# Optimization experiments

Hardware: AMD Instinct MI355X
Metric: run time of the kernel (lower is better)

## Reference

```python
import jax, jax.numpy as jnp
import numpy as np
from jax import lax

EPS = 1e-5

def conv3x3(x, w):
    # x: [B,C,H,W], w: [O,C,3,3]
    return lax.conv_general_dilated(x, w, (1, 1), ((1, 1), (1, 1)),
                                    dimension_numbers=("NCHW", "OIHW", "NCHW"))

def convbnrelu(x, w, bn):
    gamma, beta, mean, var = bn  # each [C]
    y = conv3x3(x, w)
    scale = (gamma / jnp.sqrt(var + EPS))[:, None, None]
    shift = (beta - mean * gamma / jnp.sqrt(var + EPS))[:, None, None]
    return jax.nn.relu(y * scale + shift)

def conv1x1(x, w, b):
    # w: [O,C,1,1], b: [O]
    return jnp.einsum("bchw,oc->bohw", x, w[:, :, 0, 0]) + b[:, None, None]

def pam(x, wb, bb, wc, bc, wd, bd, alpha, lfm=None):
    B, C, H, W = x.shape
    N = H * W
    q = conv1x1(x, wb, bb)
    k = conv1x1(x, wc, bc)
    v = conv1x1(x, wd, bd)
    if lfm is not None:  # VFAM: qkv flags all 1 -> multiply q, k, v
        q = q * lfm
        k = k * lfm
        v = v * lfm
    fb = q.reshape(B, -1, N).transpose(0, 2, 1)           # [B,N,Cq]
    fc = k.reshape(B, -1, N)                              # [B,Cq,N]
    attn = jax.nn.softmax(jnp.matmul(fb, fc), axis=-1)    # [B,N,N]
    fd = v.reshape(B, C, N)                               # [B,C,N]
    fe = jnp.matmul(fd, attn.transpose(0, 2, 1)).reshape(B, C, H, W)
    return alpha * fe + x

def cam(x, beta):
    B, C, H, W = x.shape
    N = H * W
    fa = x.reshape(B, C, N)
    attn = jnp.matmul(fa, fa.transpose(0, 2, 1))          # [B,C,C]
    attn = jnp.max(attn, axis=-1, keepdims=True) - attn
    attn = jax.nn.softmax(attn, axis=-1)
    fe = jnp.matmul(attn, fa).reshape(B, C, H, W)
    return beta * fe + x

def setup_inputs() -> dict:
    key = jax.random.key(0)
    ks = iter(jax.random.split(key, 64))
    B, Cin, H, W = 2, 2048, 64, 64
    Cmid = Cin // 4         # 512
    Cq = Cmid // 8          # 64
    nclass = 19

    def bn_pack(C):
        g = jnp.ones((C,)) + 0.1 * jax.random.normal(next(ks), (C,))
        b = 0.1 * jax.random.normal(next(ks), (C,))
        m = 0.1 * jax.random.normal(next(ks), (C,))
        v = jax.random.uniform(next(ks), (C,), minval=0.5, maxval=1.5)
        return jnp.stack([g, b, m, v])  # [4,C]

    def conv_w(O, I, kk):
        return jax.random.normal(next(ks), (O, I, kk, kk)) * (1.0 / np.sqrt(I * kk * kk))

    inp = {
        "x": jax.random.normal(next(ks), (B, Cin, H, W)),
        "loss_factor_map": jax.random.uniform(next(ks), (H, W)),
        "wp1": conv_w(Cmid, Cin, 3), "bnp1": bn_pack(Cmid),
        "wp2": conv_w(Cmid, Cmid, 3), "bnp2": bn_pack(Cmid),
        "wc1": conv_w(Cmid, Cin, 3), "bnc1": bn_pack(Cmid),
        "wc2": conv_w(Cmid, Cmid, 3), "bnc2": bn_pack(Cmid),
        "wv1": conv_w(Cmid, Cin, 3), "bnv1": bn_pack(Cmid),
        "wv2": conv_w(Cmid, Cmid, 3), "bnv2": bn_pack(Cmid),
        "pam_wb": conv_w(Cq, Cmid, 1), "pam_bb": jnp.zeros((Cq,)),
        "pam_wc": conv_w(Cq, Cmid, 1), "pam_bc": jnp.zeros((Cq,)),
        "pam_wd": conv_w(Cmid, Cmid, 1), "pam_bd": jnp.zeros((Cmid,)),
        "pam_alpha": 0.3 * jnp.ones((1,)),
        "cam_beta": 0.3 * jnp.ones((1,)),
        "vfam_wb": conv_w(Cq, Cmid, 1), "vfam_bb": jnp.zeros((Cq,)),
        "vfam_wc": conv_w(Cq, Cmid, 1), "vfam_bc": jnp.zeros((Cq,)),
        "vfam_wd": conv_w(Cmid, Cmid, 1), "vfam_bd": jnp.zeros((Cmid,)),
        "vfam_alpha": 0.3 * jnp.ones((1,)),
        "out_w": conv_w(nclass, Cmid, 1), "out_b": jnp.zeros((nclass,)),
        "p3_w": conv_w(nclass, Cmid, 1), "p3_b": jnp.zeros((nclass,)),
        "c3_w": conv_w(nclass, Cmid, 1), "c3_b": jnp.zeros((nclass,)),
    }
    return inp

def reference(x, loss_factor_map,
              wp1, bnp1, wp2, bnp2, wc1, bnc1, wc2, bnc2, wv1, bnv1, wv2, bnv2,
              pam_wb, pam_bb, pam_wc, pam_bc, pam_wd, pam_bd, pam_alpha,
              cam_beta,
              vfam_wb, vfam_bb, vfam_wc, vfam_bc, vfam_wd, vfam_bd, vfam_alpha,
              out_w, out_b, p3_w, p3_b, c3_w, c3_b):
    lfm = loss_factor_map[None, None, :, :]  # (1,1,H,W)
    # Position branch
    fp = convbnrelu(x, wp1, bnp1)
    fp = pam(fp, pam_wb, pam_bb, pam_wc, pam_bc, pam_wd, pam_bd, pam_alpha)
    fp = convbnrelu(fp, wp2, bnp2)
    # Channel branch
    fc = convbnrelu(x, wc1, bnc1)
    fc = cam(fc, cam_beta)
    fc = convbnrelu(fc, wc2, bnc2)
    # Visual-field branch (qkv_vfa_flag = [1,1,1])
    fv = convbnrelu(x, wv1, bnv1)
    fv = pam(fv, vfam_wb, vfam_bb, vfam_wc, vfam_bc, vfam_wd, vfam_bd, vfam_alpha, lfm=lfm)
    fv = convbnrelu(fv, wv2, bnv2)
    # Fusion + heads (Dropout in eval mode = identity)
    fusion = fp + fc + fv
    fusion_out = conv1x1(fusion, out_w, out_b)
    p_out = conv1x1(fp, p3_w, p3_b)
    c_out = conv1x1(fc, c3_w, c3_b)
    return (fusion_out, p_out, c_out)
```

## Files before the change

kernel.cpp:

```cpp
#include <hip/hip_runtime.h>

typedef unsigned short u16;
typedef short s16x8 __attribute__((ext_vector_type(8)));
typedef u16 u16x8 __attribute__((ext_vector_type(8)));
typedef u16 u16x4 __attribute__((ext_vector_type(4)));
typedef float f32x4 __attribute__((ext_vector_type(4)));

#define DEV __device__ __forceinline__

DEV float bf2f(u16 x) { unsigned v = ((unsigned)x) << 16; float f; __builtin_memcpy(&f, &v, 4); return f; }
DEV u16 f2bf(float f) { unsigned u; __builtin_memcpy(&u, &f, 4); u += 0x7FFFu + ((u >> 16) & 1u); return (u16)(u >> 16); }

DEV void gload16(const u16* g, u16* l) {
  __builtin_amdgcn_global_load_lds((const __attribute__((address_space(1))) void*)g,
                                   (__attribute__((address_space(3))) void*)l, 16, 0, 0);
}

__global__ void detect_dtype(const u16* __restrict__ x, int* __restrict__ flag) {
  int tid = threadIdx.x;
  float mx = 0.f;
  for (int i = tid; i < 4096; i += 256) mx = fmaxf(mx, fabsf(bf2f(x[i])));
  __shared__ float red[4];
  int wave = tid >> 6, lane = tid & 63;
  for (int off = 32; off; off >>= 1) mx = fmaxf(mx, __shfl_xor(mx, off));
  if (lane == 0) red[wave] = mx;
  __syncthreads();
  if (tid == 0) {
    mx = fmaxf(fmaxf(red[0], red[1]), fmaxf(red[2], red[3]));
    *flag = (mx > 1e4f) ? 1 : 0;
  }
}

struct CvBatch {
  const void* src[28];
  unsigned dstOff[28];
  unsigned n[28];
  unsigned chunkStart[29];
  int cnt;
};

__global__ __launch_bounds__(256) void convert_batch(CvBatch cb, u16* __restrict__ dstBase,
                                                     const int* __restrict__ flag) {
  const int isF = *flag;
  const unsigned bid = blockIdx.x;
  int j = 0;
  while (bid >= cb.chunkStart[j + 1]) ++j;
  const unsigned base = (bid - cb.chunkStart[j]) * 2048 + threadIdx.x * 8;
  const unsigned n = cb.n[j];
  if (base >= n) return;
  u16* dst = dstBase + cb.dstOff[j];
  const void* src = cb.src[j];
  if (base + 8 <= n) {
    u16x8 v;
    if (isF) {
      const float* f = (const float*)src;
#pragma unroll
      for (int k = 0; k < 8; ++k) v[k] = f2bf(f[base + k]);
    } else {
      v = *(const u16x8*)&((const u16*)src)[base];
    }
    *(u16x8*)&dst[base] = v;
  } else {
    for (unsigned i = base; i < n; ++i)
      dst[i] = isF ? f2bf(((const float*)src)[i]) : ((const u16*)src)[i];
  }
}

__global__ void bn_prep(const u16* __restrict__ cbn, float* __restrict__ out) {
  int w = blockIdx.x;
  const u16* bn = cbn + w * 2048;
  int c = threadIdx.x;
  float g = bf2f(bn[c]), be = bf2f(bn[512 + c]), m = bf2f(bn[1024 + c]), v = bf2f(bn[1536 + c]);
  float sc = g * rsqrtf(v + 1e-5f);
  out[w * 1024 + c] = sc;
  out[w * 1024 + 512 + c] = be - m * sc;
}

struct Repack3P { const void* src[3]; u16* dst[3]; };

__global__ __launch_bounds__(256) void repack_w3(Repack3P rp, int I, int Ishift,
                                                 const int* __restrict__ flag) {
  const int isF = *flag;
  const void* w = rp.src[blockIdx.z];
  u16* wr = rp.dst[blockIdx.z];
  size_t idx = ((size_t)blockIdx.x * 256 + threadIdx.x) * 8;
  int i0 = (int)(idx & (size_t)(I - 1));
  int t = (int)(idx >> Ishift);
  int o = t / 9, kk = t - o * 9;
  u16x8 v;
  if (isF) {
    const float* f = (const float*)w;
#pragma unroll
    for (int j = 0; j < 8; ++j) v[j] = f2bf(f[((size_t)o * I + i0 + j) * 9 + kk]);
  } else {
    const u16* bsrc = (const u16*)w;
#pragma unroll
    for (int j = 0; j < 8; ++j) v[j] = bsrc[((size_t)o * I + i0 + j) * 9 + kk];
  }
  *(u16x8*)&wr[idx] = v;
}

__global__ __launch_bounds__(256) void zero_border(u16* __restrict__ base, int CIN) {
  int p = blockIdx.x, b = blockIdx.y;
  int py, px;
  if (p < 66)       { py = 0;        px = p; }
  else if (p < 132) { py = 65;       px = p - 66; }
  else if (p < 196) { py = p - 131;  px = 0; }
  else              { py = p - 195;  px = 65; }
  u16* d = base + (((size_t)b * 66 + py) * 66 + px) * (size_t)CIN;
  for (int i = threadIdx.x * 8; i < CIN; i += 2048) {
    u16x8 z;
#pragma unroll
    for (int k = 0; k < 8; ++k) z[k] = 0;
    *(u16x8*)&d[i] = z;
  }
}

__global__ __launch_bounds__(256) void pad_nchw(const void* __restrict__ x, u16* __restrict__ xpad,
                                                const int* __restrict__ flag) {
  __shared__ u16 t[64][72];
  const int isF = *flag;
  int c0 = blockIdx.x * 64, h = blockIdx.y, b = blockIdx.z;
  int tid = threadIdx.x;
#pragma unroll
  for (int i = 0; i < 2; ++i) {
    int idx = i * 256 + tid;
    int cc = idx >> 3, ww = (idx & 7) * 8;
    size_t base = (((size_t)(b * 2048 + c0 + cc) * 64) + h) * 64 + ww;
    u16x8 v;
    if (isF) {
      const float* fx = (const float*)x;
#pragma unroll
      for (int j = 0; j < 8; ++j) v[j] = f2bf(fx[base + j]);
    } else {
      v = *(const u16x8*)&((const u16*)x)[base];
    }
    *(u16x8*)&t[cc][ww] = v;
  }
  __syncthreads();
#pragma unroll
  for (int i = 0; i < 2; ++i) {
    int idx = i * 256 + tid;
    int ww = idx >> 3, cc = (idx & 7) * 8;
    u16x8 v;
#pragma unroll
    for (int j = 0; j < 8; ++j) v[j] = t[cc + j][ww];
    *(u16x8*)&xpad[(((size_t)b * 66 + h + 1) * 66 + ww + 1) * 2048 + c0 + cc] = v;
  }
}

__global__ __launch_bounds__(256) void transpose64(const u16* __restrict__ src, u16* __restrict__ dst,
                                                   int R, int C) {
  __shared__ u16 t[64][72];
  int r0 = blockIdx.x * 64, c0 = blockIdx.y * 64;
  const u16* s = src + (size_t)blockIdx.z * R * C;
  u16* d = dst + (size_t)blockIdx.z * R * C;
  int tid = threadIdx.x;
#pragma unroll
  for (int i = 0; i < 2; ++i) {
    int idx = i * 256 + tid;
    int rr = idx >> 3, cc = (idx & 7) * 8;
    u16x8 v = *(const u16x8*)&s[(size_t)(r0 + rr) * C + c0 + cc];
    *(u16x8*)&t[rr][cc] = v;
  }
  __syncthreads();
#pragma unroll
  for (int i = 0; i < 2; ++i) {
    int idx = i * 256 + tid;
    int cc = idx >> 3, rr = (idx & 7) * 8;
    u16x8 v;
#pragma unroll
    for (int j = 0; j < 8; ++j) v[j] = t[rr + j][cc];
    *(u16x8*)&d[(size_t)(c0 + cc) * R + r0 + rr] = v;
  }
}

struct GemmP {
  const u16* A; const u16* B;
  long aBatch, bBatch;
  int M, N, K;
  u16* out; long outBatch; int ldOut;
  const u16* bias;
  const u16* rowscale;
  const u16* residual; long resBatch; int ldRes;
  const u16* alphaPtr;
  float* outF; long outFBatch;
  const u16* B2; const u16* bias2; u16* out2;
};

template <int BM, int BN, int EPI>
__global__ __launch_bounds__(256) void gemm_nt(GemmP p) {
  static_assert(EPI != 2 || BM >= BN, "EPI2 LDS bounce needs BM>=BN");
  constexpr int HB = (BM + BN) * 32;
  __shared__ __align__(16) u16 ls[2][HB];
  const int tid = threadIdx.x;
  int bz = blockIdx.z;
  const u16* Bsel = p.B;
  const u16* biasSel = p.bias;
  u16* outSel = p.out;
  if (EPI == 0 && p.out2) {
    const int h = gridDim.z >> 1;
    if (bz >= h) { bz -= h; Bsel = p.B2; biasSel = p.bias2; outSel = p.out2; }
  }
  const int m0 = blockIdx.x * BM, n0 = blockIdx.y * BN;
  const u16* A = p.A + (size_t)bz * p.aBatch;
  const u16* Bp = Bsel + (size_t)bz * p.bBatch;
  const int wave = tid >> 6, lane = tid & 63;
  const int quad = lane >> 4, r16 = lane & 15;
  const int wm = (wave >> 1) * (BM / 2), wn = (wave & 1) * (BN / 2);
  constexpr int TM = BM / 32, TN = BN / 32;
  f32x4 acc[TM][TN] = {};
  const int srow = tid >> 2, sch = (tid & 3) * 8;
  const int K = p.K;
  auto stage = [&](int buf, int k0) {
#pragma unroll
    for (int i = 0; i < BM / 64; ++i)
      gload16(&A[(size_t)(m0 + i * 64 + srow) * K + k0 + sch], &ls[buf][i * 2048 + wave * 512]);
#pragma unroll
    for (int i = 0; i < BN / 64; ++i)
      gload16(&Bp[(size_t)(n0 + i * 64 + srow) * K + k0 + sch],
              &ls[buf][BM * 32 + i * 2048 + wave * 512]);
  };
  stage(0, 0);
  __syncthreads();
  int cur = 0;
  for (int k0 = 0; k0 < K; k0 += 32) {
    if (k0 + 32 < K) stage(cur ^ 1, k0 + 32);
    const u16* lA = &ls[cur][0];
    const u16* lB = &ls[cur][BM * 32];
    s16x8 av[TM], bv[TN];
#pragma unroll
    for (int t = 0; t < TM; ++t) av[t] = *(const s16x8*)&lA[(wm + t * 16 + r16) * 32 + quad * 8];
#pragma unroll
    for (int t = 0; t < TN; ++t) bv[t] = *(const s16x8*)&lB[(wn + t * 16 + r16) * 32 + quad * 8];
#pragma unroll
    for (int i = 0; i < TM; ++i)
#pragma unroll
      for (int j = 0; j < TN; ++j)
        acc[i][j] = __builtin_amdgcn_mfma_f32_16x16x32_bf16(av[i], bv[j], acc[i][j], 0, 0, 0);
    __syncthreads();
    cur ^= 1;
  }
  if constexpr (EPI == 2) {
    float* lsF = (float*)&ls[0][0];
#pragma unroll
    for (int i = 0; i < TM; ++i) {
      __syncthreads();
#pragma unroll
      for (int j = 0; j < TN; ++j) {
        const int col = wn + j * 16 + r16;
#pragma unroll
        for (int r = 0; r < 4; ++r) {
          const int rowL = (wave >> 1) * 16 + quad * 4 + r;
          lsF[rowL * BN + col] = acc[i][j][r];
        }
      }
      __syncthreads();
      constexpr int PASSES = (32 * BN) / 1024;
#pragma unroll
      for (int pp = 0; pp < PASSES; ++pp) {
        const int lin = (pp * 256 + tid) * 4;
        const int rowL = lin / BN, col = lin & (BN - 1);
        const int gm = m0 + (rowL >> 4) * (BM / 2) + i * 16 + (rowL & 15);
        *(f32x4*)&p.outF[(size_t)bz * p.outFBatch + (size_t)gm * p.ldOut + (n0 + col)] =
            *(const f32x4*)&lsF[lin];
      }
    }
    return;
  }
  float alpha = 0.f;
  if (EPI == 3) alpha = bf2f(p.alphaPtr[0]);
#pragma unroll
  for (int i = 0; i < TM; ++i) {
#pragma unroll
    for (int j = 0; j < TN; ++j) {
      const int nn = n0 + wn + j * 16 + r16;
      float bia = 0.f;
      if ((EPI == 0 || EPI == 1) && biasSel) bia = bf2f(biasSel[nn]);
#pragma unroll
      for (int r = 0; r < 4; ++r) {
        const int mm = m0 + wm + i * 16 + quad * 4 + r;
        float v = acc[i][j][r];
        if (EPI == 0) {
          v += bia;
          if (p.rowscale) v *= bf2f(p.rowscale[mm]);
          outSel[(size_t)bz * p.outBatch + (size_t)mm * p.ldOut + nn] = f2bf(v);
        } else if (EPI == 1) {
          v += bia;
          if (p.rowscale) v *= bf2f(p.rowscale[mm]);
          p.out[(size_t)bz * p.outBatch + (size_t)nn * p.ldOut + mm] = f2bf(v);
        } else {
          float res = bf2f(p.residual[(size_t)bz * p.resBatch + (size_t)mm * p.ldRes + nn]);
          v = alpha * v + res;
          const int py = mm >> 6, px = mm & 63;
          p.out[(size_t)bz * p.outBatch + ((size_t)(py + 1) * 66 + (px + 1)) * p.ldOut + nn] = f2bf(v);
        }
      }
    }
  }
}

struct Conv3P {
  const u16* in[3];
  const u16* wr[3];
  u16* out[3];
  const float* bn;
};

template <int CIN>
__global__ __launch_bounds__(256) void conv3x3_k(Conv3P p) {
  __shared__ __align__(16) u16 ls[2][8192];
  const int tid = threadIdx.x;
  const int z = blockIdx.z, ci = z >> 1, b = z & 1;
  const int m0 = blockIdx.x * 128, n0 = blockIdx.y * 128;
  const u16* __restrict__ xin = p.in[ci];
  const u16* __restrict__ wr = p.wr[ci];
  const int wave = tid >> 6, lane = tid & 63;
  const int quad = lane >> 4, r16 = lane & 15;
  const int wm = (wave >> 1) * 64, wn = (wave & 1) * 64;
  f32x4 acc[4][4] = {};
  const int srow = tid >> 2, sch = (tid & 3) * 8;
  const int p0 = m0 + srow, p1 = p0 + 64;
  const size_t a0 = (((size_t)b * 66 + (p0 >> 6)) * 66 + (p0 & 63)) * CIN + sch;
  const size_t a1 = (((size_t)b * 66 + (p1 >> 6)) * 66 + (p1 & 63)) * CIN + sch;
  const size_t b0 = ((size_t)(n0 + srow) * 9) * CIN + sch;
  const size_t b1 = ((size_t)(n0 + 64 + srow) * 9) * CIN + sch;
  auto stage = [&](int buf, int kh, int kw, int c) {
    const size_t soff = ((size_t)(kh * 66 + kw)) * CIN + c;
    const size_t woff = (size_t)(kh * 3 + kw) * CIN + c;
    u16* base = &ls[buf][0];
    gload16(&xin[a0 + soff], base + wave * 512);
    gload16(&xin[a1 + soff], base + 2048 + wave * 512);
    gload16(&wr[b0 + woff], base + 4096 + wave * 512);
    gload16(&wr[b1 + woff], base + 6144 + wave * 512);
  };
  const int NT = (CIN / 32) * 9;
  stage(0, 0, 0, 0);
  __syncthreads();
  int cur = 0;
  int khN = 0, kwN = 1, cN = 0;
  for (int t = 0; t < NT; ++t) {
    if (t + 1 < NT) {
      stage(cur ^ 1, khN, kwN, cN);
      if (++kwN == 3) { kwN = 0; if (++khN == 3) { khN = 0; cN += 32; } }
    }
    const u16* base = &ls[cur][0];
    s16x8 av[4], bv[4];
#pragma unroll
    for (int tt = 0; tt < 4; ++tt)
      av[tt] = *(const s16x8*)&base[(wm + tt * 16 + r16) * 32 + quad * 8];
#pragma unroll
    for (int tt = 0; tt < 4; ++tt)
      bv[tt] = *(const s16x8*)&base[4096 + (wn + tt * 16 + r16) * 32 + quad * 8];
#pragma unroll
    for (int i = 0; i < 4; ++i)
#pragma unroll
      for (int j = 0; j < 4; ++j)
        acc[i][j] = __builtin_amdgcn_mfma_f32_16x16x32_bf16(av[i], bv[j], acc[i][j], 0, 0, 0);
    __syncthreads();
    cur ^= 1;
  }
  u16* __restrict__ out = p.out[ci];
  const float* bnS = p.bn + ci * 1024;
#pragma unroll
  for (int i = 0; i < 4; ++i) {
#pragma unroll
    for (int j = 0; j < 4; ++j) {
      const int nn = n0 + wn + j * 16 + r16;
      const float s = bnS[nn], sh = bnS[512 + nn];
#pragma unroll
      for (int r = 0; r < 4; ++r) {
        const int mm = m0 + wm + i * 16 + quad * 4 + r;
        float v = fmaxf(acc[i][j][r] * s + sh, 0.f);
        out[((size_t)b * 4096 + mm) * 512 + nn] = f2bf(v);
      }
    }
  }
}

__global__ __launch_bounds__(256) void softmax4096(const float* __restrict__ S, u16* __restrict__ P) {
  int row = blockIdx.x, tid = threadIdx.x;
  const float* sr = S + (size_t)row * 4096;
  f32x4 v[4];
  float mx = -3.4e38f;
#pragma unroll
  for (int i = 0; i < 4; ++i) {
    v[i] = *(const f32x4*)&sr[(i * 256 + tid) * 4];
    mx = fmaxf(mx, fmaxf(fmaxf(v[i][0], v[i][1]), fmaxf(v[i][2], v[i][3])));
  }
  __shared__ float red[8];
  int wave = tid >> 6, lane = tid & 63;
  for (int off = 32; off; off >>= 1) mx = fmaxf(mx, __shfl_xor(mx, off));
  if (lane == 0) red[wave] = mx;
  __syncthreads();
  mx = fmaxf(fmaxf(red[0], red[1]), fmaxf(red[2], red[3]));
  float sum = 0.f;
#pragma unroll
  for (int i = 0; i < 4; ++i)
#pragma unroll
    for (int j = 0; j < 4; ++j) { float e = __expf(v[i][j] - mx); v[i][j] = e; sum += e; }
  for (int off = 32; off; off >>= 1) sum += __shfl_xor(sum, off);
  if (lane == 0) red[4 + wave] = sum;
  __syncthreads();
  sum = red[4] + red[5] + red[6] + red[7];
  float inv = 1.f / sum;
  u16* pr = P + (size_t)row * 4096;
#pragma unroll
  for (int i = 0; i < 4; ++i) {
    u16x4 ov;
#pragma unroll
    for (int j = 0; j < 4; ++j) ov[j] = f2bf(v[i][j] * inv);
    *(u16x4*)&pr[(i * 256 + tid) * 4] = ov;
  }
}

__global__ __launch_bounds__(256) void softmax_cam(const float* __restrict__ S, u16* __restrict__ P) {
  int row = blockIdx.x, tid = threadIdx.x;
  const float* sr = S + (size_t)row * 512;
  float a = sr[tid], b = sr[tid + 256];
  __shared__ float red[12];
  int wave = tid >> 6, lane = tid & 63;
  float mx = fmaxf(a, b);
  for (int off = 32; off; off >>= 1) mx = fmaxf(mx, __shfl_xor(mx, off));
  if (lane == 0) red[wave] = mx;
  __syncthreads();
  float M1 = fmaxf(fmaxf(red[0], red[1]), fmaxf(red[2], red[3]));
  float mn = fminf(a, b);
  for (int off = 32; off; off >>= 1) mn = fminf(mn, __shfl_xor(mn, off));
  if (lane == 0) red[4 + wave] = mn;
  __syncthreads();
  float m2 = M1 - fminf(fminf(red[4], red[5]), fminf(red[6], red[7]));
  float e0 = __expf((M1 - a) - m2), e1 = __expf((M1 - b) - m2);
  float sum = e0 + e1;
  for (int off = 32; off; off >>= 1) sum += __shfl_xor(sum, off);
  if (lane == 0) red[8 + wave] = sum;
  __syncthreads();
  sum = red[8] + red[9] + red[10] + red[11];
  float inv = 1.f / sum;
  P[(size_t)row * 512 + tid] = f2bf(e0 * inv);
  P[(size_t)row * 512 + tid + 256] = f2bf(e1 * inv);
}

__global__ __launch_bounds__(256) void final_out_k(const u16* __restrict__ fp2, const u16* __restrict__ fc2,
                                                   const u16* __restrict__ fv2,
                                                   const u16* ow, const u16* ob, const u16* pw,
                                                   const u16* pb, const u16* cw, const u16* cb,
                                                   void* __restrict__ out, const int* __restrict__ flag) {
  __shared__ float wl[19 * 512];
  int tid = threadIdx.x, which = blockIdx.y;
  const u16* W = which == 0 ? ow : which == 1 ? pw : cw;
  const u16* Bb = which == 0 ? ob : which == 1 ? pb : cb;
  for (int i = tid; i < 19 * 512; i += 256) wl[i] = bf2f(W[i]);
  __syncthreads();
  int pix = blockIdx.x * 256 + threadIdx.x;
  size_t rb = (size_t)pix * 512;
  float acc[19];
#pragma unroll
  for (int o = 0; o < 19; ++o) acc[o] = 0.f;
  for (int c = 0; c < 512; c += 8) {
    float xs[8];
    if (which == 0) {
      u16x8 a = *(const u16x8*)&fp2[rb + c];
      u16x8 d = *(const u16x8*)&fc2[rb + c];
      u16x8 e = *(const u16x8*)&fv2[rb + c];
#pragma unroll
      for (int j = 0; j < 8; ++j) xs[j] = bf2f(a[j]) + bf2f(d[j]) + bf2f(e[j]);
    } else {
      const u16* src = which == 1 ? fp2 : fc2;
      u16x8 a = *(const u16x8*)&src[rb + c];
#pragma unroll
      for (int j = 0; j < 8; ++j) xs[j] = bf2f(a[j]);
    }
#pragma unroll
    for (int o = 0; o < 19; ++o) {
      const float* wv = &wl[o * 512 + c];
#pragma unroll
      for (int j = 0; j < 8; ++j) acc[o] += xs[j] * wv[j];
    }
  }
  int b = pix >> 12, n = pix & 4095;
  const int isF32 = *flag;
#pragma unroll
  for (int o = 0; o < 19; ++o) {
    size_t idx = (size_t)which * 155648 + ((size_t)(b * 19 + o)) * 4096 + n;
    float v = acc[o] + bf2f(Bb[o]);
    if (isF32) ((float*)out)[idx] = v;
    else ((u16*)out)[idx] = f2bf(v);
  }
}

static const size_t OFF_XPAD  = 0;
static const size_t OFF_WR1A  = 35684352;
static const size_t OFF_WR1B  = 54558720;
static const size_t OFF_WR1C  = 73433088;
static const size_t OFF_ARENA = 92307456;
static const size_t OFF_S     = 0;
static const size_t OFF_P     = 67108864;
static const size_t OFF_FP1   = 125861888;
static const size_t OFF_FC1   = 134250496;
static const size_t OFF_FV1   = 142639104;
static const size_t OFF_FC1T  = 151027712;
static const size_t OFF_QT    = 159416320;
static const size_t OFF_KT    = 160464896;
static const size_t OFF_VT    = 161513472;
static const size_t OFF_WRSA  = 151027712;
static const size_t OFF_WRSB  = 155746304;
static const size_t OFF_WRSC  = 161513472;
static const size_t OFF_PADP  = 169902080;
static const size_t OFF_PADC  = 178823168;
static const size_t OFF_PADV  = 187744256;
static const size_t OFF_FP2   = 125861888;
static const size_t OFF_FC2   = 134250496;
static const size_t OFF_FV2   = 142639104;
static const size_t OFF_SC    = 196665344;
static const size_t OFF_PC    = 198762496;
static const size_t OFF_BN    = 199811072;
static const size_t OFF_FLAG  = 199835648;
static const size_t OFF_SMALL = 199835904;
static const size_t SO_CBN    = 0;
static const size_t SO_PWB    = 12288;
static const size_t SO_PBB    = 45056;
static const size_t SO_PWC    = 45120;
static const size_t SO_PBC    = 77888;
static const size_t SO_PWD    = 77952;
static const size_t SO_PBD    = 340096;
static const size_t SO_PAL    = 340608;
static const size_t SO_CBETA  = 340624;
static const size_t SO_VWB    = 340640;
static const size_t SO_VBB    = 373408;
static const size_t SO_VWC    = 373472;
static const size_t SO_VBC    = 406240;
static const size_t SO_VWD    = 406304;
static const size_t SO_VBD    = 668448;
static const size_t SO_VAL    = 668960;
static const size_t SO_OW     = 668976;
static const size_t SO_OB     = 678704;
static const size_t SO_PW3    = 678736;
static const size_t SO_PB3    = 688464;
static const size_t SO_CW3    = 688496;
static const size_t SO_CB3    = 698224;
static const size_t SO_LFM    = 698256;
static const size_t SO_END    = 702352;
static const size_t WS_NEEDED = OFF_SMALL + SO_END * 2;

extern "C" void kernel_launch(void* const* d_in, const int* in_sizes, int n_in,
                              void* d_out, int out_size, void* d_ws, size_t ws_size,
                              hipStream_t stream) {
  if (ws_size < WS_NEEDED) return;
  (void)in_sizes; (void)n_in; (void)out_size;

  char* ws = (char*)d_ws;
  u16* xpad   = (u16*)(ws + OFF_XPAD);
  u16* wr1a   = (u16*)(ws + OFF_WR1A);
  u16* wr1b   = (u16*)(ws + OFF_WR1B);
  u16* wr1c   = (u16*)(ws + OFF_WR1C);
  float* S    = (float*)(ws + OFF_S);
  u16* P      = (u16*)(ws + OFF_P);
  u16* fp1    = (u16*)(ws + OFF_FP1);
  u16* fc1    = (u16*)(ws + OFF_FC1);
  u16* fv1    = (u16*)(ws + OFF_FV1);
  u16* fc1T   = (u16*)(ws + OFF_FC1T);
  u16* qt     = (u16*)(ws + OFF_QT);
  u16* kt     = (u16*)(ws + OFF_KT);
  u16* vT     = (u16*)(ws + OFF_VT);
  u16* wrsa   = (u16*)(ws + OFF_WRSA);
  u16* wrsb   = (u16*)(ws + OFF_WRSB);
  u16* wrsc   = (u16*)(ws + OFF_WRSC);
  u16* padP   = (u16*)(ws + OFF_PADP);
  u16* padC   = (u16*)(ws + OFF_PADC);
  u16* padV   = (u16*)(ws + OFF_PADV);
  u16* fp2    = (u16*)(ws + OFF_FP2);
  u16* fc2    = (u16*)(ws + OFF_FC2);
  u16* fv2    = (u16*)(ws + OFF_FV2);
  float* Sc   = (float*)(ws + OFF_SC);
  u16* Pc     = (u16*)(ws + OFF_PC);
  float* bnb  = (float*)(ws + OFF_BN);
  int* flag   = (int*)(ws + OFF_FLAG);
  u16* sm     = (u16*)(ws + OFF_SMALL);

  detect_dtype<<<1, 256, 0, stream>>>((const u16*)d_in[0], flag);
  {
    CvBatch cb{};
    int jn = 0; unsigned chunks = 0;
    auto addJob = [&](int i, size_t dstOff, unsigned n) {
      cb.src[jn] = d_in[i]; cb.dstOff[jn] = (unsigned)dstOff; cb.n[jn] = n;
      cb.chunkStart[jn] = chunks; chunks += (n + 2047) / 2048; ++jn;
    };
    addJob(3,  SO_CBN + 0 * 2048, 2048);
    addJob(7,  SO_CBN + 1 * 2048, 2048);
    addJob(11, SO_CBN + 2 * 2048, 2048);
    addJob(5,  SO_CBN + 3 * 2048, 2048);
    addJob(9,  SO_CBN + 4 * 2048, 2048);
    addJob(13, SO_CBN + 5 * 2048, 2048);
    addJob(14, SO_PWB, 32768);  addJob(15, SO_PBB, 64);
    addJob(16, SO_PWC, 32768);  addJob(17, SO_PBC, 64);
    addJob(18, SO_PWD, 262144); addJob(19, SO_PBD, 512);
    addJob(20, SO_PAL, 1);      addJob(21, SO_CBETA, 1);
    addJob(22, SO_VWB, 32768);  addJob(23, SO_VBB, 64);
    addJob(24, SO_VWC, 32768);  addJob(25, SO_VBC, 64);
    addJob(26, SO_VWD, 262144); addJob(27, SO_VBD, 512);
    addJob(28, SO_VAL, 1);
    addJob(29, SO_OW, 9728);    addJob(30, SO_OB, 19);
    addJob(31, SO_PW3, 9728);   addJob(32, SO_PB3, 19);
    addJob(33, SO_CW3, 9728);   addJob(34, SO_CB3, 19);
    addJob(1,  SO_LFM, 4096);
    cb.cnt = jn; cb.chunkStart[jn] = chunks;
    convert_batch<<<chunks, 256, 0, stream>>>(cb, sm, flag);
  }

  bn_prep<<<6, 512, 0, stream>>>(sm + SO_CBN, bnb);

  zero_border<<<dim3(260, 2), 256, 0, stream>>>(xpad, 2048);
  pad_nchw<<<dim3(32, 64, 2), 256, 0, stream>>>(d_in[0], xpad, flag);

  {
    Repack3P rp{};
    rp.src[0] = d_in[2];  rp.dst[0] = wr1a;
    rp.src[1] = d_in[6];  rp.dst[1] = wr1b;
    rp.src[2] = d_in[10]; rp.dst[2] = wr1c;
    repack_w3<<<dim3(4608, 1, 3), 256, 0, stream>>>(rp, 2048, 11, flag);
  }
  {
    Conv3P c{};
    c.in[0] = xpad; c.in[1] = xpad; c.in[2] = xpad;
    c.wr[0] = wr1a; c.wr[1] = wr1b; c.wr[2] = wr1c;
    c.out[0] = fp1; c.out[1] = fc1; c.out[2] = fv1;
    c.bn = bnb;
    conv3x3_k<2048><<<dim3(32, 4, 6), 256, 0, stream>>>(c);
  }

  auto runPam = [&](const u16* src, const u16* wb, const u16* bb, const u16* wck, const u16* bck,
                    const u16* wd, const u16* bd, const u16* alphaP, const u16* rs, u16* padOut) {
    GemmP g{};
    g.A = src; g.aBatch = 2097152; g.B = wb; g.bBatch = 0; g.M = 4096; g.N = 64; g.K = 512;
    g.out = qt; g.outBatch = 262144; g.ldOut = 64; g.bias = bb; g.rowscale = rs;
    g.B2 = wck; g.bias2 = bck; g.out2 = kt;
    gemm_nt<64, 64, 0><<<dim3(64, 1, 4), 256, 0, stream>>>(g);
    GemmP gv{};
    gv.A = src; gv.aBatch = 2097152; gv.B = wd; gv.bBatch = 0; gv.M = 4096; gv.N = 512; gv.K = 512;
    gv.out = vT; gv.outBatch = 2097152; gv.ldOut = 4096; gv.bias = bd; gv.rowscale = rs;
    gemm_nt<64, 128, 1><<<dim3(64, 4, 2), 256, 0, stream>>>(gv);
    zero_border<<<dim3(260, 2), 256, 0, stream>>>(padOut, 512);
    for (int b = 0; b < 2; ++b) {
      GemmP gs{};
      gs.A = qt + (size_t)b * 262144; gs.B = kt + (size_t)b * 262144;
      gs.M = 4096; gs.N = 4096; gs.K = 64;
      gs.outF = S; gs.outFBatch = 0; gs.ldOut = 4096;
      gemm_nt<128, 128, 2><<<dim3(32, 32, 1), 256, 0, stream>>>(gs);
      softmax4096<<<4096, 256, 0, stream>>>(S, P);
      GemmP gf{};
      gf.A = P; gf.aBatch = 0; gf.B = vT + (size_t)b * 2097152; gf.bBatch = 0;
      gf.M = 4096; gf.N = 512; gf.K = 4096;
      gf.out = padOut + (size_t)b * 2230272; gf.outBatch = 0; gf.ldOut = 512;
      gf.residual = src + (size_t)b * 2097152; gf.resBatch = 0; gf.ldRes = 512;
      gf.alphaPtr = alphaP;
      gemm_nt<128, 64, 3><<<dim3(32, 8, 1), 256, 0, stream>>>(gf);
    }
  };
  runPam(fp1, sm + SO_PWB, sm + SO_PBB, sm + SO_PWC, sm + SO_PBC, sm + SO_PWD, sm + SO_PBD,
         sm + SO_PAL, nullptr, padP);
  runPam(fv1, sm + SO_VWB, sm + SO_VBB, sm + SO_VWC, sm + SO_VBC, sm + SO_VWD, sm + SO_VBD,
         sm + SO_VAL, sm + SO_LFM, padV);

  transpose64<<<dim3(64, 8, 2), 256, 0, stream>>>(fc1, fc1T, 4096, 512);
  {
    GemmP g{};
    g.A = fc1T; g.aBatch = 2097152; g.B = fc1T; g.bBatch = 2097152;
    g.M = 512; g.N = 512; g.K = 4096;
    g.outF = Sc; g.outFBatch = 262144; g.ldOut = 512;
    gemm_nt<64, 64, 2><<<dim3(8, 8, 2), 256, 0, stream>>>(g);
  }
  softmax_cam<<<1024, 256, 0, stream>>>(Sc, Pc);
  zero_border<<<dim3(260, 2), 256, 0, stream>>>(padC, 512);
  {
    GemmP g{};
    g.A = fc1; g.aBatch = 2097152; g.B = Pc; g.bBatch = 262144;
    g.M = 4096; g.N = 512; g.K = 512;
    g.out = padC; g.outBatch = 2230272; g.ldOut = 512;
    g.residual = fc1; g.resBatch = 2097152; g.ldRes = 512;
    g.alphaPtr = sm + SO_CBETA;
    gemm_nt<128, 128, 3><<<dim3(32, 4, 2), 256, 0, stream>>>(g);
  }

  {
    Repack3P rp{};
    rp.src[0] = d_in[4];  rp.dst[0] = wrsa;
    rp.src[1] = d_in[8];  rp.dst[1] = wrsb;
    rp.src[2] = d_in[12]; rp.dst[2] = wrsc;
    repack_w3<<<dim3(1152, 1, 3), 256, 0, stream>>>(rp, 512, 9, flag);
  }
  {
    Conv3P c{};
    c.in[0] = padP; c.in[1] = padC; c.in[2] = padV;
    c.wr[0] = wrsa; c.wr[1] = wrsb; c.wr[2] = wrsc;
    c.out[0] = fp2; c.out[1] = fc2; c.out[2] = fv2;
    c.bn = bnb + 3 * 1024;
    conv3x3_k<512><<<dim3(32, 4, 6), 256, 0, stream>>>(c);
  }

  final_out_k<<<dim3(32, 3), 256, 0, stream>>>(fp2, fc2, fv2, sm + SO_OW, sm + SO_OB,
                                               sm + SO_PW3, sm + SO_PB3, sm + SO_CW3, sm + SO_CB3,
                                               d_out, flag);
}
```

Before: 1.508 ms.

## Triple-buffer conv3x3 loads, stage weight repack through LDS, retile PAM output GEMM

The 3x3 convolution kernel moves from a double-buffered LDS pipeline to a triple-buffered one. Explicit vmcnt waits and raw barriers let two tiles of global-to-LDS loads stay in flight while MFMAs run. The weight repack kernel now gives each output channel its own block, reads the contiguous 9*I weights into shared memory with coalesced loads, and writes the transposed layout from LDS, replacing the strided global gathers. The PAM attention-times-value GEMM switches to 64x64 tiles, doubling the block count for better occupancy at the cost of less reuse per block.

Result: no change. 1.500 ms (-0.5%).

```diff
diff --git a/kernel.cpp b/kernel.cpp
--- a/kernel.cpp
+++ b/kernel.cpp
@@ -78,26 +78,37 @@
 
 struct Repack3P { const void* src[3]; u16* dst[3]; };
 
-__global__ __launch_bounds__(256) void repack_w3(Repack3P rp, int I, int Ishift,
+__global__ __launch_bounds__(256) void repack_w3(Repack3P rp, int I, int logI,
                                                  const int* __restrict__ flag) {
+  __shared__ u16 t9[9 * 2048];
   const int isF = *flag;
+  const int o = blockIdx.x;
   const void* w = rp.src[blockIdx.z];
   u16* wr = rp.dst[blockIdx.z];
-  size_t idx = ((size_t)blockIdx.x * 256 + threadIdx.x) * 8;
-  int i0 = (int)(idx & (size_t)(I - 1));
-  int t = (int)(idx >> Ishift);
-  int o = t / 9, kk = t - o * 9;
-  u16x8 v;
+  const int n9 = 9 * I;
+  const size_t ibase = (size_t)o * n9;
+  const int tid = threadIdx.x;
   if (isF) {
-    const float* f = (const float*)w;
-#pragma unroll
-    for (int j = 0; j < 8; ++j) v[j] = f2bf(f[((size_t)o * I + i0 + j) * 9 + kk]);
+    const float* f = (const float*)w + ibase;
+    for (int x = tid * 8; x < n9; x += 2048) {
+      u16x8 v;
+#pragma unroll
+      for (int j = 0; j < 8; ++j) v[j] = f2bf(f[x + j]);
+      *(u16x8*)&t9[x] = v;
+    }
   } else {
-    const u16* bsrc = (const u16*)w;
-#pragma unroll
-    for (int j = 0; j < 8; ++j) v[j] = bsrc[((size_t)o * I + i0 + j) * 9 + kk];
-  }
-  *(u16x8*)&wr[idx] = v;
+    const u16* s = (const u16*)w + ibase;
+    for (int x = tid * 8; x < n9; x += 2048) *(u16x8*)&t9[x] = *(const u16x8*)&s[x];
+  }
+  __syncthreads();
+  u16* dst = wr + ibase;
+  for (int v = tid * 8; v < n9; v += 2048) {
+    const int kk = v >> logI, i = v & (I - 1);
+    u16x8 ov;
+#pragma unroll
+    for (int j = 0; j < 8; ++j) ov[j] = t9[(i + j) * 9 + kk];
+    *(u16x8*)&dst[v] = ov;
+  }
 }
 
 __global__ __launch_bounds__(256) void zero_border(u16* __restrict__ base, int CIN) {
@@ -309,7 +320,7 @@
 
 template <int CIN>
 __global__ __launch_bounds__(256) void conv3x3_k(Conv3P p) {
-  __shared__ __align__(16) u16 ls[2][8192];
+  __shared__ __align__(16) u16 ls[3][8192];
   const int tid = threadIdx.x;
   const int z = blockIdx.z, ci = z >> 1, b = z & 1;
   const int m0 = blockIdx.x * 128, n0 = blockIdx.y * 128;
@@ -336,14 +347,16 @@
   };
   const int NT = (CIN / 32) * 9;
   stage(0, 0, 0, 0);
-  __syncthreads();
+  stage(1, 0, 1, 0);
+  stage(2, 0, 2, 0);
   int cur = 0;
-  int khN = 0, kwN = 1, cN = 0;
+  int khN = 1, kwN = 0, cN = 0;
   for (int t = 0; t < NT; ++t) {
-    if (t + 1 < NT) {
-      stage(cur ^ 1, khN, kwN, cN);
-      if (++kwN == 3) { kwN = 0; if (++khN == 3) { khN = 0; cN += 32; } }
-    }
+    if (t < NT - 2)       asm volatile("s_waitcnt vmcnt(8)" ::: "memory");
+    else if (t == NT - 2) asm volatile("s_waitcnt vmcnt(4)" ::: "memory");
+    else                  asm volatile("s_waitcnt vmcnt(0)" ::: "memory");
+    __builtin_amdgcn_s_barrier();
+    __builtin_amdgcn_sched_barrier(0);
     const u16* base = &ls[cur][0];
     s16x8 av[4], bv[4];
 #pragma unroll
@@ -357,8 +370,13 @@
 #pragma unroll
       for (int j = 0; j < 4; ++j)
         acc[i][j] = __builtin_amdgcn_mfma_f32_16x16x32_bf16(av[i], bv[j], acc[i][j], 0, 0, 0);
-    __syncthreads();
-    cur ^= 1;
+    __builtin_amdgcn_sched_barrier(0);
+    __builtin_amdgcn_s_barrier();
+    if (t + 3 < NT) {
+      stage(cur, khN, kwN, cN);
+      if (++kwN == 3) { kwN = 0; if (++khN == 3) { khN = 0; cN += 32; } }
+    }
+    if (++cur == 3) cur = 0;
   }
   u16* __restrict__ out = p.out[ci];
   const float* bnS = p.bn + ci * 1024;
@@ -618,7 +636,7 @@
     rp.src[0] = d_in[2];  rp.dst[0] = wr1a;
     rp.src[1] = d_in[6];  rp.dst[1] = wr1b;
     rp.src[2] = d_in[10]; rp.dst[2] = wr1c;
-    repack_w3<<<dim3(4608, 1, 3), 256, 0, stream>>>(rp, 2048, 11, flag);
+    repack_w3<<<dim3(512, 1, 3), 256, 0, stream>>>(rp, 2048, 11, flag);
   }
   {
     Conv3P c{};
@@ -654,7 +672,7 @@
       gf.out = padOut + (size_t)b * 2230272; gf.outBatch = 0; gf.ldOut = 512;
       gf.residual = src + (size_t)b * 2097152; gf.resBatch = 0; gf.ldRes = 512;
       gf.alphaPtr = alphaP;
-      gemm_nt<128, 64, 3><<<dim3(32, 8, 1), 256, 0, stream>>>(gf);
+      gemm_nt<64, 64, 3><<<dim3(64, 8, 1), 256, 0, stream>>>(gf);
     }
   };
   runPam(fp1, sm + SO_PWB, sm + SO_PBB, sm + SO_PWC, sm + SO_PBC, sm + SO_PWD, sm + SO_PBD,
@@ -687,7 +705,7 @@
     rp.src[0] = d_in[4];  rp.dst[0] = wrsa;
     rp.src[1] = d_in[8];  rp.dst[1] = wrsb;
     rp.src[2] = d_in[12]; rp.dst[2] = wrsc;
-    repack_w3<<<dim3(1152, 1, 3), 256, 0, stream>>>(rp, 512, 9, flag);
+    repack_w3<<<dim3(512, 1, 3), 256, 0, stream>>>(rp, 512, 9, flag);
   }
   {
     Conv3P c{};
```
